# Kernel tuning notes

Measured on AMD Instinct MI355X. Metric: run time of the kernel, lower is better.

Reference implementation:

```python
import jax, jax.numpy as jnp
import numpy as np

B, S, D, K, T = 8, 1024, 128, 16, 8  # batch, seq_len, dim, stack_size, recursion depth
N = B * S                            # per-token stack memory batch
RESIDUAL = 0.1                       # cfg.RESIDUAL_WEIGHT
EPS = 1e-6                           # cfg.EPSILON
SCALE = D ** -0.5


def _clinear(zr, zi, Wr, Wi):
    # (zr + i*zi) @ (Wr + i*Wi); W stored [in, out] (torch Linear weight transposed)
    return zr @ Wr - zi @ Wi, zi @ Wr + zr @ Wi


def _cattn(zr, zi, p):
    # ComplexAttention: complex q/k/v, softmax over concat([real, imag]) scores
    Wqr, Wqi, Wkr, Wki, Wvr, Wvi = p
    qr, qi = _clinear(zr, zi, Wqr, Wqi)
    kr, ki = _clinear(zr, zi, Wkr, Wki)
    vr, vi = _clinear(zr, zi, Wvr, Wvi)
    qf = jnp.concatenate([qr, qi], -1)
    kf = jnp.concatenate([kr, ki], -1)
    a = jax.nn.softmax(jnp.einsum('...id,...jd->...ij', qf, kf) * SCALE, -1)
    return jnp.einsum('...ij,...jd->...id', a, vr), jnp.einsum('...ij,...jd->...id', a, vi)


def setup_inputs() -> dict:
    key = jax.random.key(0)
    ks = jax.random.split(key, 18)
    mk = lambda k: jax.random.normal(k, (D, D), jnp.float32) * (D ** -0.5)
    inp = {
        'x_real': jax.random.normal(ks[0], (B, S, D), jnp.float32),
        'x_imag': jax.random.normal(ks[1], (B, S, D), jnp.float32),
        # sequence ComplexAttention weights
        'Wq_r': mk(ks[2]), 'Wq_i': mk(ks[3]),
        'Wk_r': mk(ks[4]), 'Wk_i': mk(ks[5]),
        'Wv_r': mk(ks[6]), 'Wv_i': mk(ks[7]),
        # stack-memory ComplexAttention weights
        'Mq_r': mk(ks[8]), 'Mq_i': mk(ks[9]),
        'Mk_r': mk(ks[10]), 'Mk_i': mk(ks[11]),
        'Mv_r': mk(ks[12]), 'Mv_i': mk(ks[13]),
        # ctrl projection (push/pop/stay logits) and output modulus projection
        'Wc': jax.random.normal(ks[14], (2 * D, 3), jnp.float32) * 0.05,
        'bc': jnp.zeros((3,), jnp.float32),
        'Wo': jax.random.normal(ks[15], (2 * D, D), jnp.float32) * ((2 * D) ** -0.5),
        'bo': jnp.zeros((D,), jnp.float32),
    }
    return inp


def reference(x_real, x_imag, Wq_r, Wq_i, Wk_r, Wk_i, Wv_r, Wv_i,
              Mq_r, Mq_i, Mk_r, Mk_i, Mv_r, Mv_i, Wc, bc, Wo, bo):
    seq_p = (Wq_r, Wq_i, Wk_r, Wk_i, Wv_r, Wv_i)
    mem_p = (Mq_r, Mq_i, Mk_r, Mk_i, Mv_r, Mv_i)
    mem0 = jnp.zeros((N, K, 2 * D), x_real.dtype)
    ptr0 = jnp.zeros((N, K), x_real.dtype).at[:, 0].set(1.0)  # pointer starts at slot 0

    def step(carry, _):
        zr, zi, mem, ptr = carry
        ar, ai = _cattn(zr, zi, seq_p)                         # [B,S,D] complex attention
        zf = jnp.concatenate([ar.reshape(N, D), ai.reshape(N, D)], -1)  # [N,2D]
        # gated push/pop/stay (sigmoid, then normalized as in DifferentiableStackMemory)
        g = jax.nn.sigmoid(zf @ Wc + bc)                       # [N,3]
        tot = g.sum(-1, keepdims=True) + EPS
        push, pop, stay = g[:, 0:1] / tot, g[:, 1:2] / tot, g[:, 2:3] / tot
        new_ptr = push * jnp.roll(ptr, 1, 1) + pop * jnp.roll(ptr, -1, 1) + stay * ptr
        mem = mem * (1.0 - push[..., None]) + push[..., None] * zf[:, None, :]  # gated write
        mr, mi = _cattn(mem[..., :D], mem[..., D:], mem_p)     # attention over K stack slots
        read = (jnp.concatenate([mr, mi], -1) * new_ptr[..., None]).sum(1)      # pointer-weighted read [N,2D]
        zr2 = ar + RESIDUAL * read[:, :D].reshape(B, S, D)
        zi2 = ai + RESIDUAL * read[:, D:].reshape(B, S, D)
        return (zr2, zi2, mem, new_ptr), None

    (zr, zi, _, _), _ = jax.lax.scan(step, (x_real, x_imag, mem0, ptr0), None, length=T)
    # ComplexModulusProjection: Linear(2*dim -> dim) on concat([real, imag])
    return jnp.concatenate([zr, zi], -1) @ Wo + bo
```

## Files before the change

### kernel.cpp

```cpp
#include <hip/hip_runtime.h>
#include <stdint.h>

typedef __attribute__((ext_vector_type(4))) float f32x4;

constexpr float QK_SCALE = 0.08838834764831845f;


__global__ void k_init32(const float* __restrict__ xr, const float* __restrict__ xi,
                         float* __restrict__ Z, float* __restrict__ Mm,
                         float* __restrict__ PSUM){
  for (int i = blockIdx.x*blockDim.x + threadIdx.x; i < 8192*256; i += gridDim.x*blockDim.x){
    int n = i >> 8, d = i & 255;
    Z[i]  = (d < 128) ? xr[n*128 + d] : xi[n*128 + d - 128];
    Mm[i] = 0.f;
    if (i < 8192) PSUM[i] = 1.f;
  }
}

template<int EPI>
__launch_bounds__(256, 2)
__global__ void k_gemm32(const float* __restrict__ A, int nb,
                         const float* __restrict__ W0r, const float* __restrict__ W0i,
                         const float* __restrict__ W1r, const float* __restrict__ W1i,
                         const float* __restrict__ W2r, const float* __restrict__ W2i,
                         float* __restrict__ C, const float* __restrict__ PSUM,
                         const float* __restrict__ bias){
  __shared__ float As[32][132];
  __shared__ float Bs[32][132];
  const int bx = blockIdx.x % nb, by = blockIdx.x / nb;
  const int m0 = by << 7, n0 = bx << 7;
  const int tid = threadIdx.x;
  const int tx = tid & 15, ty = tid >> 4;
  const float* Wr = W0r; const float* Wi = W0i;
  if constexpr (EPI == 0){
    int sec = n0 >> 8;
    Wr = (sec == 0) ? W0r : (sec == 1) ? W1r : W2r;
    Wi = (sec == 0) ? W0i : (sec == 1) ? W1i : W2i;
  }
  const int hn = (n0 >> 7) & 1;
  float acc[8][8];
  #pragma unroll
  for (int i = 0; i < 8; ++i)
    #pragma unroll
    for (int j = 0; j < 8; ++j) acc[i][j] = 0.f;

  for (int kt = 0; kt < 8; ++kt){
    if (kt) __syncthreads();
    #pragma unroll
    for (int i = 0; i < 4; ++i){
      int c = i*256 + tid;
      int row = c >> 3, k4 = c & 7;
      f32x4 v = *(const f32x4*)&A[(size_t)(m0 + row)*256 + kt*32 + k4*4];
      As[k4*4+0][row] = v.x; As[k4*4+1][row] = v.y;
      As[k4*4+2][row] = v.z; As[k4*4+3][row] = v.w;
    }
    #pragma unroll
    for (int i = 0; i < 4; ++i){
      int c = i*256 + tid;
      int k = c >> 5, n4 = c & 31;
      int gk = kt*32 + k;
      f32x4 v;
      if constexpr (EPI == 2){
        v = *(const f32x4*)&W0r[(size_t)gk*128 + n4*4];
      } else {
        int hk = gk >> 7, kk = gk & 127;
        const float* src = ((hk ^ hn) == 0) ? Wr : Wi;
        v = *(const f32x4*)&src[(size_t)kk*128 + n4*4];
        if (hk == 1 && hn == 0){ v.x = -v.x; v.y = -v.y; v.z = -v.z; v.w = -v.w; }
      }
      *(f32x4*)&Bs[k][n4*4] = v;
    }
    __syncthreads();
    #pragma unroll 8
    for (int k = 0; k < 32; ++k){
      float a[8], b[8];
      *(f32x4*)&a[0] = *(const f32x4*)&As[k][ty*8];
      *(f32x4*)&a[4] = *(const f32x4*)&As[k][ty*8 + 4];
      *(f32x4*)&b[0] = *(const f32x4*)&Bs[k][tx*8];
      *(f32x4*)&b[4] = *(const f32x4*)&Bs[k][tx*8 + 4];
      #pragma unroll
      for (int i = 0; i < 8; ++i)
        #pragma unroll
        for (int j = 0; j < 8; ++j) acc[i][j] += a[i]*b[j];
    }
  }
  #pragma unroll
  for (int i = 0; i < 8; ++i){
    const int row = m0 + ty*8 + i;
    const int col = n0 + tx*8;
    if constexpr (EPI == 0){
      *(f32x4*)&C[(size_t)row*768 + col]     = *(const f32x4*)&acc[i][0];
      *(f32x4*)&C[(size_t)row*768 + col + 4] = *(const f32x4*)&acc[i][4];
    } else if constexpr (EPI == 1){
      const float s = 0.1f * PSUM[row];
      f32x4 z0 = *(const f32x4*)&C[(size_t)row*256 + col];
      f32x4 z1 = *(const f32x4*)&C[(size_t)row*256 + col + 4];
      z0.x += s*acc[i][0]; z0.y += s*acc[i][1]; z0.z += s*acc[i][2]; z0.w += s*acc[i][3];
      z1.x += s*acc[i][4]; z1.y += s*acc[i][5]; z1.z += s*acc[i][6]; z1.w += s*acc[i][7];
      *(f32x4*)&C[(size_t)row*256 + col]     = z0;
      *(f32x4*)&C[(size_t)row*256 + col + 4] = z1;
    } else {
      f32x4 b0 = *(const f32x4*)&bias[col];
      f32x4 b1 = *(const f32x4*)&bias[col + 4];
      f32x4 o0 = {acc[i][0]+b0.x, acc[i][1]+b0.y, acc[i][2]+b0.z, acc[i][3]+b0.w};
      f32x4 o1 = {acc[i][4]+b1.x, acc[i][5]+b1.y, acc[i][6]+b1.z, acc[i][7]+b1.w};
      *(f32x4*)&C[(size_t)row*128 + col]     = o0;
      *(f32x4*)&C[(size_t)row*128 + col + 4] = o1;
    }
  }
}

__launch_bounds__(512, 1)
__global__ void k_attn32(const float* __restrict__ QKV, float* __restrict__ ZF,
                         float* __restrict__ Mm, float* __restrict__ PSUM,
                         const float* __restrict__ Wc, const float* __restrict__ bc){
  __shared__ __align__(16) float QTc[16][36];
  __shared__ __align__(16) float KV[16*260];
  __shared__ __align__(16) float Ps[32*260];
  const int tid = threadIdx.x;
  const int tx = tid & 63;
  const int ty = tid >> 6;
  const int batch = blockIdx.x >> 5, qt = blockIdx.x & 31;
  const int nbase = batch*1024 + qt*32;
  const int kv0 = batch*1024;

  float O[4][4];
  #pragma unroll
  for (int r = 0; r < 4; ++r)
    #pragma unroll
    for (int j = 0; j < 4; ++j) O[r][j] = 0.f;
  float mr[4] = {-3.0e30f, -3.0e30f, -3.0e30f, -3.0e30f};
  float lr[4] = {0.f, 0.f, 0.f, 0.f};

  const int qq = tid & 31, qd = tid >> 5;

  for (int t = 0; t < 4; ++t){
    const int kb = kv0 + t*256;
    float S[4][4];
    #pragma unroll
    for (int r = 0; r < 4; ++r)
      #pragma unroll
      for (int e = 0; e < 4; ++e) S[r][e] = 0.f;

    for (int dc = 0; dc < 16; ++dc){
      __syncthreads();
      QTc[qd][qq] = QKV[(size_t)(nbase + qq)*768 + dc*16 + qd];
      #pragma unroll
      for (int i = 0; i < 2; ++i){
        const int c = i*512 + tid;
        const int key = c & 255, d4 = c >> 8;
        f32x4 v = *(const f32x4*)&QKV[(size_t)(kb + key)*768 + 256 + dc*16 + d4*4];
        KV[(d4*4+0)*260 + key] = v.x; KV[(d4*4+1)*260 + key] = v.y;
        KV[(d4*4+2)*260 + key] = v.z; KV[(d4*4+3)*260 + key] = v.w;
      }
      __syncthreads();
      #pragma unroll
      for (int k = 0; k < 16; ++k){
        const f32x4 a = *(const f32x4*)&QTc[k][ty*4];
        const f32x4 b = *(const f32x4*)&KV[k*260 + tx*4];
        S[0][0] += a.x*b.x; S[0][1] += a.x*b.y; S[0][2] += a.x*b.z; S[0][3] += a.x*b.w;
        S[1][0] += a.y*b.x; S[1][1] += a.y*b.y; S[1][2] += a.y*b.z; S[1][3] += a.y*b.w;
        S[2][0] += a.z*b.x; S[2][1] += a.z*b.y; S[2][2] += a.z*b.z; S[2][3] += a.z*b.w;
        S[3][0] += a.w*b.x; S[3][1] += a.w*b.y; S[3][2] += a.w*b.z; S[3][3] += a.w*b.w;
      }
    }
    #pragma unroll
    for (int r = 0; r < 4; ++r){
      #pragma unroll
      for (int e = 0; e < 4; ++e) S[r][e] *= QK_SCALE;
      float tm = fmaxf(fmaxf(S[r][0], S[r][1]), fmaxf(S[r][2], S[r][3]));
      tm = fmaxf(tm, __shfl_xor(tm, 1));
      tm = fmaxf(tm, __shfl_xor(tm, 2));
      tm = fmaxf(tm, __shfl_xor(tm, 4));
      tm = fmaxf(tm, __shfl_xor(tm, 8));
      tm = fmaxf(tm, __shfl_xor(tm, 16));
      tm = fmaxf(tm, __shfl_xor(tm, 32));
      const float mn = fmaxf(mr[r], tm);
      const float al = expf(mr[r] - mn);
      float p0 = expf(S[r][0] - mn), p1 = expf(S[r][1] - mn);
      float p2 = expf(S[r][2] - mn), p3 = expf(S[r][3] - mn);
      float rs = (p0 + p1) + (p2 + p3);
      rs += __shfl_xor(rs, 1); rs += __shfl_xor(rs, 2);
      rs += __shfl_xor(rs, 4); rs += __shfl_xor(rs, 8);
      rs += __shfl_xor(rs, 16); rs += __shfl_xor(rs, 32);
      lr[r] = lr[r]*al + rs;
      mr[r] = mn;
      O[r][0] *= al; O[r][1] *= al; O[r][2] *= al; O[r][3] *= al;
      f32x4 w = {p0, p1, p2, p3};
      *(f32x4*)&Ps[(ty*4 + r)*260 + tx*4] = w;
    }
    for (int ks = 0; ks < 16; ++ks){
      __syncthreads();
      #pragma unroll
      for (int i = 0; i < 2; ++i){
        const int c = i*512 + tid;
        const int key = c >> 6, d4 = c & 63;
        *(f32x4*)&KV[key*260 + d4*4] =
            *(const f32x4*)&QKV[(size_t)(kb + ks*16 + key)*768 + 512 + d4*4];
      }
      __syncthreads();
      #pragma unroll
      for (int kg = 0; kg < 4; ++kg){
        const f32x4 P0 = *(const f32x4*)&Ps[(ty*4+0)*260 + ks*16 + kg*4];
        const f32x4 P1 = *(const f32x4*)&Ps[(ty*4+1)*260 + ks*16 + kg*4];
        const f32x4 P2 = *(const f32x4*)&Ps[(ty*4+2)*260 + ks*16 + kg*4];
        const f32x4 P3 = *(const f32x4*)&Ps[(ty*4+3)*260 + ks*16 + kg*4];
        #pragma unroll
        for (int k2 = 0; k2 < 4; ++k2){
          const f32x4 v = *(const f32x4*)&KV[(kg*4+k2)*260 + tx*4];
          const float a0 = P0[k2], a1 = P1[k2], a2 = P2[k2], a3 = P3[k2];
          O[0][0] += a0*v.x; O[0][1] += a0*v.y; O[0][2] += a0*v.z; O[0][3] += a0*v.w;
          O[1][0] += a1*v.x; O[1][1] += a1*v.y; O[1][2] += a1*v.z; O[1][3] += a1*v.w;
          O[2][0] += a2*v.x; O[2][1] += a2*v.y; O[2][2] += a2*v.z; O[2][3] += a2*v.w;
          O[3][0] += a3*v.x; O[3][1] += a3*v.y; O[3][2] += a3*v.z; O[3][3] += a3*v.w;
        }
      }
    }
  }
  const float bc0 = bc[0], bc1 = bc[1], bc2 = bc[2];
  #pragma unroll
  for (int r = 0; r < 4; ++r){
    const float inv = 1.f / lr[r];
    #pragma unroll
    for (int j = 0; j < 4; ++j) O[r][j] *= inv;
    float d0 = 0.f, d1 = 0.f, d2 = 0.f;
    #pragma unroll
    for (int j = 0; j < 4; ++j){
      const int dim = tx*4 + j;
      const float z = O[r][j];
      d0 += z*Wc[dim*3 + 0]; d1 += z*Wc[dim*3 + 1]; d2 += z*Wc[dim*3 + 2];
    }
    d0 += __shfl_xor(d0,1); d0 += __shfl_xor(d0,2); d0 += __shfl_xor(d0,4);
    d0 += __shfl_xor(d0,8); d0 += __shfl_xor(d0,16); d0 += __shfl_xor(d0,32);
    d1 += __shfl_xor(d1,1); d1 += __shfl_xor(d1,2); d1 += __shfl_xor(d1,4);
    d1 += __shfl_xor(d1,8); d1 += __shfl_xor(d1,16); d1 += __shfl_xor(d1,32);
    d2 += __shfl_xor(d2,1); d2 += __shfl_xor(d2,2); d2 += __shfl_xor(d2,4);
    d2 += __shfl_xor(d2,8); d2 += __shfl_xor(d2,16); d2 += __shfl_xor(d2,32);
    const float g0 = 1.f/(1.f + expf(-(d0 + bc0)));
    const float g1 = 1.f/(1.f + expf(-(d1 + bc1)));
    const float g2 = 1.f/(1.f + expf(-(d2 + bc2)));
    const float tt = g0 + g1 + g2, tot = tt + 1e-6f;
    const float push = g0/tot;
    const int row = nbase + ty*4 + r;
    if (tx == 0) PSUM[row] *= tt/tot;
    const size_t idx = (size_t)row*256 + tx*4;
    f32x4 z0 = {O[r][0], O[r][1], O[r][2], O[r][3]};
    f32x4 m0 = *(const f32x4*)&Mm[idx];
    m0.x += push*(z0.x - m0.x); m0.y += push*(z0.y - m0.y);
    m0.z += push*(z0.z - m0.z); m0.w += push*(z0.w - m0.w);
    *(f32x4*)&Mm[idx] = m0;
    *(f32x4*)&ZF[idx] = z0;
  }
}

extern "C" void kernel_launch(void* const* d_in, const int* in_sizes, int n_in,
                              void* d_out, int out_size, void* d_ws, size_t ws_size,
                              hipStream_t stream){
  (void)in_sizes; (void)n_in; (void)out_size; (void)ws_size;
  const float* xr   = (const float*)d_in[0];
  const float* xi   = (const float*)d_in[1];
  const float* Wq_r = (const float*)d_in[2];
  const float* Wq_i = (const float*)d_in[3];
  const float* Wk_r = (const float*)d_in[4];
  const float* Wk_i = (const float*)d_in[5];
  const float* Wv_r = (const float*)d_in[6];
  const float* Wv_i = (const float*)d_in[7];
  const float* Mv_r = (const float*)d_in[12];
  const float* Mv_i = (const float*)d_in[13];
  const float* Wc   = (const float*)d_in[14];
  const float* bc   = (const float*)d_in[15];
  const float* Wo   = (const float*)d_in[16];
  const float* bo   = (const float*)d_in[17];

  uint8_t* w = (uint8_t*)d_ws;
  float* Z    = (float*)w; w += (size_t)8192*256*4;
  float* QKV  = (float*)w; w += (size_t)8192*768*4;
  float* Mm   = (float*)w; w += (size_t)8192*256*4;
  float* PSUM = (float*)w; w += (size_t)8192*4;
  float* ZF   = Z;

  k_init32<<<dim3(1024), dim3(256), 0, stream>>>(xr, xi, Z, Mm, PSUM);
  for (int t = 0; t < 8; ++t){
    k_gemm32<0><<<dim3(384), dim3(256), 0, stream>>>(Z, 6,
        Wq_r, Wq_i, Wk_r, Wk_i, Wv_r, Wv_i, QKV, nullptr, nullptr);
    k_attn32<<<dim3(256), dim3(512), 0, stream>>>(QKV, ZF, Mm, PSUM, Wc, bc);
    k_gemm32<1><<<dim3(128), dim3(256), 0, stream>>>(Mm, 2,
        Mv_r, Mv_i, nullptr, nullptr, nullptr, nullptr, Z, PSUM, nullptr);
  }
  k_gemm32<2><<<dim3(64), dim3(256), 0, stream>>>(Z, 1,
      Wo, nullptr, nullptr, nullptr, nullptr, nullptr, (float*)d_out, nullptr, bo);
}
```

Baseline: 2.503 ms.

## Keep Q and softmax probabilities in registers via readlane; halve GEMM row tiles

Measured after the change: 2.112 ms, median of 2. -15.6%, faster.

```diff
diff --git a/kernel.cpp b/kernel.cpp
--- a/kernel.cpp
+++ b/kernel.cpp
@@ -4,6 +4,14 @@
 typedef __attribute__((ext_vector_type(4))) float f32x4;
 
 constexpr float QK_SCALE = 0.08838834764831845f;
+
+#define DEV static __device__ __forceinline__
+
+DEV float rdl(float v, int l){
+  union { float f; int i; } u; u.f = v;
+  u.i = __builtin_amdgcn_readlane(u.i, l);
+  return u.f;
+}
 
 
 __global__ void k_init32(const float* __restrict__ xr, const float* __restrict__ xi,
@@ -17,7 +25,7 @@
   }
 }
 
-template<int EPI>
+template<int EPI, int BM>
 __launch_bounds__(256, 2)
 __global__ void k_gemm32(const float* __restrict__ A, int nb,
                          const float* __restrict__ W0r, const float* __restrict__ W0i,
@@ -25,10 +33,11 @@
                          const float* __restrict__ W2r, const float* __restrict__ W2i,
                          float* __restrict__ C, const float* __restrict__ PSUM,
                          const float* __restrict__ bias){
-  __shared__ float As[32][132];
+  constexpr int RM = BM / 16;
+  __shared__ float As[32][BM + 4];
   __shared__ float Bs[32][132];
   const int bx = blockIdx.x % nb, by = blockIdx.x / nb;
-  const int m0 = by << 7, n0 = bx << 7;
+  const int m0 = by * BM, n0 = bx << 7;
   const int tid = threadIdx.x;
   const int tx = tid & 15, ty = tid >> 4;
   const float* Wr = W0r; const float* Wi = W0i;
@@ -38,16 +47,16 @@
     Wi = (sec == 0) ? W0i : (sec == 1) ? W1i : W2i;
   }
   const int hn = (n0 >> 7) & 1;
-  float acc[8][8];
-  #pragma unroll
-  for (int i = 0; i < 8; ++i)
+  float acc[RM][8];
+  #pragma unroll
+  for (int i = 0; i < RM; ++i)
     #pragma unroll
     for (int j = 0; j < 8; ++j) acc[i][j] = 0.f;
 
   for (int kt = 0; kt < 8; ++kt){
     if (kt) __syncthreads();
     #pragma unroll
-    for (int i = 0; i < 4; ++i){
+    for (int i = 0; i < BM/32; ++i){
       int c = i*256 + tid;
       int row = c >> 3, k4 = c & 7;
       f32x4 v = *(const f32x4*)&A[(size_t)(m0 + row)*256 + kt*32 + k4*4];
@@ -73,20 +82,21 @@
     __syncthreads();
     #pragma unroll 8
     for (int k = 0; k < 32; ++k){
-      float a[8], b[8];
-      *(f32x4*)&a[0] = *(const f32x4*)&As[k][ty*8];
-      *(f32x4*)&a[4] = *(const f32x4*)&As[k][ty*8 + 4];
+      float a[RM], b[8];
+      #pragma unroll
+      for (int i4 = 0; i4 < RM/4; ++i4)
+        *(f32x4*)&a[i4*4] = *(const f32x4*)&As[k][ty*RM + i4*4];
       *(f32x4*)&b[0] = *(const f32x4*)&Bs[k][tx*8];
       *(f32x4*)&b[4] = *(const f32x4*)&Bs[k][tx*8 + 4];
       #pragma unroll
-      for (int i = 0; i < 8; ++i)
+      for (int i = 0; i < RM; ++i)
         #pragma unroll
         for (int j = 0; j < 8; ++j) acc[i][j] += a[i]*b[j];
     }
   }
   #pragma unroll
-  for (int i = 0; i < 8; ++i){
-    const int row = m0 + ty*8 + i;
+  for (int i = 0; i < RM; ++i){
+    const int row = m0 + ty*RM + i;
     const int col = n0 + tx*8;
     if constexpr (EPI == 0){
       *(f32x4*)&C[(size_t)row*768 + col]     = *(const f32x4*)&acc[i][0];
@@ -114,9 +124,7 @@
 __global__ void k_attn32(const float* __restrict__ QKV, float* __restrict__ ZF,
                          float* __restrict__ Mm, float* __restrict__ PSUM,
                          const float* __restrict__ Wc, const float* __restrict__ bc){
-  __shared__ __align__(16) float QTc[16][36];
   __shared__ __align__(16) float KV[16*260];
-  __shared__ __align__(16) float Ps[32*260];
   const int tid = threadIdx.x;
   const int tx = tid & 63;
   const int ty = tid >> 6;
@@ -124,6 +132,13 @@
   const int nbase = batch*1024 + qt*32;
   const int kv0 = batch*1024;
 
+  float qreg[4][4];
+  #pragma unroll
+  for (int r = 0; r < 4; ++r)
+    #pragma unroll
+    for (int g = 0; g < 4; ++g)
+      qreg[r][g] = QKV[(size_t)(nbase + ty*4 + r)*768 + g*64 + tx];
+
   float O[4][4];
   #pragma unroll
   for (int r = 0; r < 4; ++r)
@@ -132,8 +147,6 @@
   float mr[4] = {-3.0e30f, -3.0e30f, -3.0e30f, -3.0e30f};
   float lr[4] = {0.f, 0.f, 0.f, 0.f};
 
-  const int qq = tid & 31, qd = tid >> 5;
-
   for (int t = 0; t < 4; ++t){
     const int kb = kv0 + t*256;
     float S[4][4];
@@ -142,28 +155,36 @@
       #pragma unroll
       for (int e = 0; e < 4; ++e) S[r][e] = 0.f;
 
-    for (int dc = 0; dc < 16; ++dc){
-      __syncthreads();
-      QTc[qd][qq] = QKV[(size_t)(nbase + qq)*768 + dc*16 + qd];
-      #pragma unroll
-      for (int i = 0; i < 2; ++i){
-        const int c = i*512 + tid;
-        const int key = c & 255, d4 = c >> 8;
-        f32x4 v = *(const f32x4*)&QKV[(size_t)(kb + key)*768 + 256 + dc*16 + d4*4];
-        KV[(d4*4+0)*260 + key] = v.x; KV[(d4*4+1)*260 + key] = v.y;
-        KV[(d4*4+2)*260 + key] = v.z; KV[(d4*4+3)*260 + key] = v.w;
+    #pragma unroll
+    for (int gg = 0; gg < 4; ++gg){
+      for (int dcc = 0; dcc < 4; ++dcc){
+        const int dc = gg*4 + dcc;
+        __syncthreads();
+        #pragma unroll
+        for (int i = 0; i < 2; ++i){
+          const int c = i*512 + tid;
+          const int key = c & 255, d4 = c >> 8;
+          f32x4 v = *(const f32x4*)&QKV[(size_t)(kb + key)*768 + 256 + dc*16 + d4*4];
+          KV[(d4*4+0)*260 + key] = v.x; KV[(d4*4+1)*260 + key] = v.y;
+          KV[(d4*4+2)*260 + key] = v.z; KV[(d4*4+3)*260 + key] = v.w;
+        }
+        __syncthreads();
+        #pragma unroll
+        for (int k = 0; k < 16; ++k){
+          const int ln = dcc*16 + k;
+          const float a0 = rdl(qreg[0][gg], ln);
+          const float a1 = rdl(qreg[1][gg], ln);
+          const float a2 = rdl(qreg[2][gg], ln);
+          const float a3 = rdl(qreg[3][gg], ln);
+          const f32x4 b = *(const f32x4*)&KV[k*260 + tx*4];
+          S[0][0] += a0*b.x; S[0][1] += a0*b.y; S[0][2] += a0*b.z; S[0][3] += a0*b.w;
+          S[1][0] += a1*b.x; S[1][1] += a1*b.y; S[1][2] += a1*b.z; S[1][3] += a1*b.w;
+          S[2][0] += a2*b.x; S[2][1] += a2*b.y; S[2][2] += a2*b.z; S[2][3] += a2*b.w;
+          S[3][0] += a3*b.x; S[3][1] += a3*b.y; S[3][2] += a3*b.z; S[3][3] += a3*b.w;
+        }
       }
-      __syncthreads();
-      #pragma unroll
-      for (int k = 0; k < 16; ++k){
-        const f32x4 a = *(const f32x4*)&QTc[k][ty*4];
-        const f32x4 b = *(const f32x4*)&KV[k*260 + tx*4];
-        S[0][0] += a.x*b.x; S[0][1] += a.x*b.y; S[0][2] += a.x*b.z; S[0][3] += a.x*b.w;
-        S[1][0] += a.y*b.x; S[1][1] += a.y*b.y; S[1][2] += a.y*b.z; S[1][3] += a.y*b.w;
-        S[2][0] += a.z*b.x; S[2][1] += a.z*b.y; S[2][2] += a.z*b.z; S[2][3] += a.z*b.w;
-        S[3][0] += a.w*b.x; S[3][1] += a.w*b.y; S[3][2] += a.w*b.z; S[3][3] += a.w*b.w;
-      }
-    }
+    }
+    float pp[4][4];
     #pragma unroll
     for (int r = 0; r < 4; ++r){
       #pragma unroll
@@ -177,17 +198,15 @@
       tm = fmaxf(tm, __shfl_xor(tm, 32));
       const float mn = fmaxf(mr[r], tm);
       const float al = expf(mr[r] - mn);
-      float p0 = expf(S[r][0] - mn), p1 = expf(S[r][1] - mn);
-      float p2 = expf(S[r][2] - mn), p3 = expf(S[r][3] - mn);
-      float rs = (p0 + p1) + (p2 + p3);
+      pp[r][0] = expf(S[r][0] - mn); pp[r][1] = expf(S[r][1] - mn);
+      pp[r][2] = expf(S[r][2] - mn); pp[r][3] = expf(S[r][3] - mn);
+      float rs = (pp[r][0] + pp[r][1]) + (pp[r][2] + pp[r][3]);
       rs += __shfl_xor(rs, 1); rs += __shfl_xor(rs, 2);
       rs += __shfl_xor(rs, 4); rs += __shfl_xor(rs, 8);
       rs += __shfl_xor(rs, 16); rs += __shfl_xor(rs, 32);
       lr[r] = lr[r]*al + rs;
       mr[r] = mn;
       O[r][0] *= al; O[r][1] *= al; O[r][2] *= al; O[r][3] *= al;
-      f32x4 w = {p0, p1, p2, p3};
-      *(f32x4*)&Ps[(ty*4 + r)*260 + tx*4] = w;
     }
     for (int ks = 0; ks < 16; ++ks){
       __syncthreads();
@@ -201,14 +220,14 @@
       __syncthreads();
       #pragma unroll
       for (int kg = 0; kg < 4; ++kg){
-        const f32x4 P0 = *(const f32x4*)&Ps[(ty*4+0)*260 + ks*16 + kg*4];
-        const f32x4 P1 = *(const f32x4*)&Ps[(ty*4+1)*260 + ks*16 + kg*4];
-        const f32x4 P2 = *(const f32x4*)&Ps[(ty*4+2)*260 + ks*16 + kg*4];
-        const f32x4 P3 = *(const f32x4*)&Ps[(ty*4+3)*260 + ks*16 + kg*4];
+        const int ln = ks*4 + kg;
         #pragma unroll
         for (int k2 = 0; k2 < 4; ++k2){
+          const float a0 = rdl(pp[0][k2], ln);
+          const float a1 = rdl(pp[1][k2], ln);
+          const float a2 = rdl(pp[2][k2], ln);
+          const float a3 = rdl(pp[3][k2], ln);
           const f32x4 v = *(const f32x4*)&KV[(kg*4+k2)*260 + tx*4];
-          const float a0 = P0[k2], a1 = P1[k2], a2 = P2[k2], a3 = P3[k2];
           O[0][0] += a0*v.x; O[0][1] += a0*v.y; O[0][2] += a0*v.z; O[0][3] += a0*v.w;
           O[1][0] += a1*v.x; O[1][1] += a1*v.y; O[1][2] += a1*v.z; O[1][3] += a1*v.w;
           O[2][0] += a2*v.x; O[2][1] += a2*v.y; O[2][2] += a2*v.z; O[2][3] += a2*v.w;
@@ -281,12 +300,12 @@
 
   k_init32<<<dim3(1024), dim3(256), 0, stream>>>(xr, xi, Z, Mm, PSUM);
   for (int t = 0; t < 8; ++t){
-    k_gemm32<0><<<dim3(384), dim3(256), 0, stream>>>(Z, 6,
+    k_gemm32<0,64><<<dim3(768), dim3(256), 0, stream>>>(Z, 6,
         Wq_r, Wq_i, Wk_r, Wk_i, Wv_r, Wv_i, QKV, nullptr, nullptr);
     k_attn32<<<dim3(256), dim3(512), 0, stream>>>(QKV, ZF, Mm, PSUM, Wc, bc);
-    k_gemm32<1><<<dim3(128), dim3(256), 0, stream>>>(Mm, 2,
+    k_gemm32<1,64><<<dim3(256), dim3(256), 0, stream>>>(Mm, 2,
         Mv_r, Mv_i, nullptr, nullptr, nullptr, nullptr, Z, PSUM, nullptr);
   }
-  k_gemm32<2><<<dim3(64), dim3(256), 0, stream>>>(Z, 1,
+  k_gemm32<2,128><<<dim3(64), dim3(256), 0, stream>>>(Z, 1,
       Wo, nullptr, nullptr, nullptr, nullptr, nullptr, (float*)d_out, nullptr, bo);
 }
```
